# Performance work log

Measured on AMD Instinct MI355X. Metric: run time of the kernel, lower is better.

The kernel has to match this reference:

```python
import jax, jax.numpy as jnp
import numpy as np

IN_FEATURES = 2048
OUT_FEATURES = 2048
ORDER = 8
BATCH = 8192


def setup_inputs() -> dict:
    key = jax.random.key(0)
    k1, k2, k3, k4 = jax.random.split(key, 4)
    x = jax.random.normal(k1, (BATCH, IN_FEATURES), dtype=jnp.float32)
    v = jax.random.normal(k2, (ORDER, max(IN_FEATURES, OUT_FEATURES)), dtype=jnp.float32)
    d = jax.random.normal(k3, (min(IN_FEATURES, OUT_FEATURES),), dtype=jnp.float32)
    bias = jax.random.normal(k4, (OUT_FEATURES,), dtype=jnp.float32) * 0.01
    return {"x": x, "v": v, "d": d, "bias": bias}


def reference(x, v, d, bias):
    # Normalize each reflection vector (row-wise L2 norm), as in the torch module.
    n = v.shape[1]  # max_feature = 2048
    vn = v / jnp.linalg.norm(v, axis=1, keepdims=True)
    # Householder matrices H_i = I - 2 v_i v_i^T, shape [order, n, n]
    H = jnp.eye(n, dtype=x.dtype)[None, :, :] - 2.0 * jnp.einsum('ab,ac->abc', vn, vn)
    # Chain multiply u = H_0 @ H_1 @ ... @ H_{order-1} (order is a small static constant)
    u = H[0]
    for i in range(1, H.shape[0]):
        u = u @ H[i]
    # out_features <= in_features branch: W = u @ (eye(in, out) @ diag(d))
    # eye(in, out) @ diag(d) places d on the leading diagonal of an [in, out] matrix,
    # so W = u[:, :out] * d (column scaling) -- same math, no dense diag matmul.
    W = u[:, :OUT_FEATURES] * d[None, :]
    y = x @ W + bias[None, :]
    return y
```

## Files before the change

kernel.cpp:

```cpp
#include <hip/hip_runtime.h>

#define N_FEAT 2048
#define ORDER 8
#define BATCH 8192
#define BLOCK 256
#define WPB 4

typedef float v4f __attribute__((ext_vector_type(4)));

__device__ __forceinline__ float dot4(v4f a, v4f b) {
    return a.x * b.x + a.y * b.y + a.z * b.z + a.w * b.w;
}

__global__ __launch_bounds__(BLOCK) void prep_kernel(
    const float* __restrict__ v, float* __restrict__ vn) {
    const int tid = threadIdx.x;
    const int lane = tid & 63, wid = tid >> 6;

    v4f a0[ORDER], a1[ORDER];
    #pragma unroll
    for (int i = 0; i < ORDER; ++i) {
        a0[i] = *(const v4f*)(v + (size_t)i * N_FEAT + tid * 4);
        a1[i] = *(const v4f*)(v + (size_t)i * N_FEAT + 1024 + tid * 4);
    }
    float ss[ORDER];
    #pragma unroll
    for (int i = 0; i < ORDER; ++i)
        ss[i] = dot4(a0[i], a0[i]) + dot4(a1[i], a1[i]);
    #pragma unroll
    for (int o = 32; o > 0; o >>= 1)
        #pragma unroll
        for (int i = 0; i < ORDER; ++i) ss[i] += __shfl_down(ss[i], o, 64);

    __shared__ float red[4][ORDER];
    if (lane == 0) {
        #pragma unroll
        for (int i = 0; i < ORDER; ++i) red[wid][i] = ss[i];
    }
    __syncthreads();
    #pragma unroll
    for (int i = 0; i < ORDER; ++i) {
        const float inv = 1.0f / sqrtf(red[0][i] + red[1][i] + red[2][i] + red[3][i]);
        *(v4f*)(vn + (size_t)i * N_FEAT + tid * 4) = a0[i] * inv;
        *(v4f*)(vn + (size_t)i * N_FEAT + 1024 + tid * 4) = a1[i] * inv;
    }
}

__global__ __launch_bounds__(BLOCK) void orth_apply_kernel(
    const float* __restrict__ x, const float* __restrict__ vn,
    const float* __restrict__ d, const float* __restrict__ bias,
    float* __restrict__ y) {
    const int tid = threadIdx.x;
    const int lane = tid & 63, wid = tid >> 6;
    const int row = blockIdx.x * WPB + wid;
    const size_t base = (size_t)row * N_FEAT;
    const int col = lane * 4;

    v4f z[8];
    #pragma unroll
    for (int c = 0; c < 8; ++c)
        z[c] = *(const v4f*)(x + base + c * 256 + col);

    #pragma unroll
    for (int i = 0; i < ORDER; ++i) {
        const float* vr = vn + (size_t)i * N_FEAT;
        v4f a[8];
        #pragma unroll
        for (int c = 0; c < 8; ++c)
            a[c] = *(const v4f*)(vr + c * 256 + col);

        float p = 0.f;
        #pragma unroll
        for (int c = 0; c < 8; ++c) p += dot4(z[c], a[c]);
        #pragma unroll
        for (int o = 1; o < 64; o <<= 1) p += __shfl_xor(p, o, 64);

        const float s = -2.0f * p;
        #pragma unroll
        for (int c = 0; c < 8; ++c) z[c] += s * a[c];
    }

    #pragma unroll
    for (int c = 0; c < 8; ++c) {
        const v4f dd = *(const v4f*)(d + c * 256 + col);
        const v4f bb = *(const v4f*)(bias + c * 256 + col);
        v4f o = z[c] * dd + bb;
        __builtin_nontemporal_store(o, (v4f*)(y + base + c * 256 + col));
    }
}

extern "C" void kernel_launch(void* const* d_in, const int* in_sizes, int n_in,
                              void* d_out, int out_size, void* d_ws, size_t ws_size,
                              hipStream_t stream) {
    const float* x    = (const float*)d_in[0];
    const float* v    = (const float*)d_in[1];
    const float* d    = (const float*)d_in[2];
    const float* bias = (const float*)d_in[3];
    float* y  = (float*)d_out;
    float* vn = (float*)d_ws;

    prep_kernel<<<1, BLOCK, 0, stream>>>(v, vn);
    orth_apply_kernel<<<BATCH / WPB, BLOCK, 0, stream>>>(x, vn, d, bias, y);
}
```

Measured before the change: 131.7 us.

## Apply Householder chain via compact WY form with batched reductions

Precomputes the Gram matrix of normalized reflection vectors and a triangular T factor in the prep kernel. The apply kernel then computes all eight projections of each row at once, reduces them together across the wavefront, and applies a single combined update. This removes the serial dependency of eight separate reduce-then-update steps per row, at the cost of reading the reflection vectors twice and a small per-row triangular combine.

```diff
diff --git a/kernel.cpp b/kernel.cpp
--- a/kernel.cpp
+++ b/kernel.cpp
@@ -13,7 +13,7 @@
 }
 
 __global__ __launch_bounds__(BLOCK) void prep_kernel(
-    const float* __restrict__ v, float* __restrict__ vn) {
+    const float* __restrict__ v, float* __restrict__ vn, float* __restrict__ Tout) {
     const int tid = threadIdx.x;
     const int lane = tid & 63, wid = tid >> 6;
 
@@ -27,29 +27,68 @@
     #pragma unroll
     for (int i = 0; i < ORDER; ++i)
         ss[i] = dot4(a0[i], a0[i]) + dot4(a1[i], a1[i]);
+    float pr[28];
     #pragma unroll
-    for (int o = 32; o > 0; o >>= 1)
+    for (int i = 0, c = 0; i < ORDER; ++i)
+        #pragma unroll
+        for (int j = i + 1; j < ORDER; ++j, ++c)
+            pr[c] = dot4(a0[i], a0[j]) + dot4(a1[i], a1[j]);
+
+    #pragma unroll
+    for (int o = 32; o > 0; o >>= 1) {
         #pragma unroll
         for (int i = 0; i < ORDER; ++i) ss[i] += __shfl_down(ss[i], o, 64);
-
-    __shared__ float red[4][ORDER];
+        #pragma unroll
+        for (int c = 0; c < 28; ++c) pr[c] += __shfl_down(pr[c], o, 64);
+    }
+    __shared__ float rss[4][ORDER];
+    __shared__ float rpr[4][28];
     if (lane == 0) {
         #pragma unroll
-        for (int i = 0; i < ORDER; ++i) red[wid][i] = ss[i];
+        for (int i = 0; i < ORDER; ++i) rss[wid][i] = ss[i];
+        #pragma unroll
+        for (int c = 0; c < 28; ++c) rpr[wid][c] = pr[c];
     }
     __syncthreads();
+
+    float inv[ORDER];
     #pragma unroll
     for (int i = 0; i < ORDER; ++i) {
-        const float inv = 1.0f / sqrtf(red[0][i] + red[1][i] + red[2][i] + red[3][i]);
-        *(v4f*)(vn + (size_t)i * N_FEAT + tid * 4) = a0[i] * inv;
-        *(v4f*)(vn + (size_t)i * N_FEAT + 1024 + tid * 4) = a1[i] * inv;
+        inv[i] = 1.0f / sqrtf(rss[0][i] + rss[1][i] + rss[2][i] + rss[3][i]);
+        *(v4f*)(vn + (size_t)i * N_FEAT + tid * 4) = a0[i] * inv[i];
+        *(v4f*)(vn + (size_t)i * N_FEAT + 1024 + tid * 4) = a1[i] * inv[i];
+    }
+
+    if (tid == 0) {
+        float G[ORDER][ORDER];
+        for (int i = 0, c = 0; i < ORDER; ++i) {
+            G[i][i] = 1.0f;
+            for (int j = i + 1; j < ORDER; ++j, ++c) {
+                float g = (rpr[0][c] + rpr[1][c] + rpr[2][c] + rpr[3][c]) * inv[i] * inv[j];
+                G[i][j] = g; G[j][i] = g;
+            }
+        }
+        float T[ORDER][ORDER];
+        for (int i = 0; i < ORDER; ++i)
+            for (int j = 0; j < ORDER; ++j) T[i][j] = 0.f;
+        T[0][0] = 2.0f;
+        for (int k = 1; k < ORDER; ++k) {
+            for (int j = 0; j < k; ++j) {
+                float s = 0.f;
+                for (int m = j; m < k; ++m) s += T[j][m] * G[m][k];
+                T[j][k] = -2.0f * s;
+            }
+            T[k][k] = 2.0f;
+        }
+        for (int i = 0; i < ORDER; ++i)
+            for (int j = 0; j < ORDER; ++j) Tout[i * ORDER + j] = T[i][j];
     }
 }
 
 __global__ __launch_bounds__(BLOCK) void orth_apply_kernel(
     const float* __restrict__ x, const float* __restrict__ vn,
-    const float* __restrict__ d, const float* __restrict__ bias,
-    float* __restrict__ y) {
+    const float* __restrict__ T, const float* __restrict__ d,
+    const float* __restrict__ bias, float* __restrict__ y) {
     const int tid = threadIdx.x;
     const int lane = tid & 63, wid = tid >> 6;
     const int row = blockIdx.x * WPB + wid;
@@ -61,23 +100,42 @@
     for (int c = 0; c < 8; ++c)
         z[c] = *(const v4f*)(x + base + c * 256 + col);
 
+    float p[ORDER];
     #pragma unroll
     for (int i = 0; i < ORDER; ++i) {
         const float* vr = vn + (size_t)i * N_FEAT;
-        v4f a[8];
+        float s0 = 0.f, s1 = 0.f, s2 = 0.f, s3 = 0.f;
+        #pragma unroll
+        for (int c = 0; c < 8; c += 4) {
+            s0 += dot4(z[c + 0], *(const v4f*)(vr + (c + 0) * 256 + col));
+            s1 += dot4(z[c + 1], *(const v4f*)(vr + (c + 1) * 256 + col));
+            s2 += dot4(z[c + 2], *(const v4f*)(vr + (c + 2) * 256 + col));
+            s3 += dot4(z[c + 3], *(const v4f*)(vr + (c + 3) * 256 + col));
+        }
+        p[i] = (s0 + s1) + (s2 + s3);
+    }
+
+    #pragma unroll
+    for (int o = 1; o < 64; o <<= 1)
+        #pragma unroll
+        for (int i = 0; i < ORDER; ++i) p[i] += __shfl_xor(p[i], o, 64);
+
+    float q[ORDER];
+    #pragma unroll
+    for (int j = 0; j < ORDER; ++j) {
+        float s = 0.f;
+        #pragma unroll
+        for (int i = 0; i <= j; ++i) s += p[i] * T[i * ORDER + j];
+        q[j] = -s;
+    }
+
+    #pragma unroll
+    for (int j = 0; j < ORDER; ++j) {
+        const float* vr = vn + (size_t)j * N_FEAT;
+        const float qj = q[j];
         #pragma unroll
         for (int c = 0; c < 8; ++c)
-            a[c] = *(const v4f*)(vr + c * 256 + col);
-
-        float p = 0.f;
-        #pragma unroll
-        for (int c = 0; c < 8; ++c) p += dot4(z[c], a[c]);
-        #pragma unroll
-        for (int o = 1; o < 64; o <<= 1) p += __shfl_xor(p, o, 64);
-
-        const float s = -2.0f * p;
-        #pragma unroll
-        for (int c = 0; c < 8; ++c) z[c] += s * a[c];
+            z[c] += qj * *(const v4f*)(vr + c * 256 + col);
     }
 
     #pragma unroll
@@ -98,7 +156,8 @@
     const float* bias = (const float*)d_in[3];
     float* y  = (float*)d_out;
     float* vn = (float*)d_ws;
+    float* T  = vn + ORDER * N_FEAT;
 
-    prep_kernel<<<1, BLOCK, 0, stream>>>(v, vn);
-    orth_apply_kernel<<<BATCH / WPB, BLOCK, 0, stream>>>(x, vn, d, bias, y);
+    prep_kernel<<<1, BLOCK, 0, stream>>>(v, vn, T);
+    orth_apply_kernel<<<BATCH / WPB, BLOCK, 0, stream>>>(x, vn, T, d, bias, y);
 }
```

New measurement: 143.4 us. 1.09x slower.
